# Performance work log

Measured on AMD Instinct MI355X. Metric: run time of the kernel, lower is better.

## Reference

```python
import jax, jax.numpy as jnp
import numpy as np

VOCAB = 50257
HID = 1024


def setup_inputs() -> dict:
    key = jax.random.key(0)
    ks = jax.random.split(key, 9)
    s = 0.05  # weight scale for numerical sanity
    return {
        "input": jax.random.randint(ks[0], (1,), 0, VOCAB),
        "hidden": jax.random.normal(ks[1], (1, 1, HID), jnp.float32),
        "emb": jax.random.normal(ks[2], (VOCAB, HID), jnp.float32) * s,
        "w_ih": jax.random.normal(ks[3], (3 * HID, HID), jnp.float32) * s,
        "w_hh": jax.random.normal(ks[4], (3 * HID, HID), jnp.float32) * s,
        "b_ih": jax.random.normal(ks[5], (3 * HID,), jnp.float32) * s,
        "b_hh": jax.random.normal(ks[6], (3 * HID,), jnp.float32) * s,
        "w_out": jax.random.normal(ks[7], (VOCAB, HID), jnp.float32) * s,
        "b_out": jax.random.normal(ks[8], (VOCAB,), jnp.float32) * s,
    }


def reference(input, hidden, emb, w_ih, w_hh, b_ih, b_hh, w_out, b_out):
    # embedding lookup -> [1, HID], then ReLU
    x = jnp.maximum(emb[input[0]], 0.0)[None, :]          # [1, H]
    h = hidden[0]                                         # [1, H] (layer 0)
    # PyTorch GRU cell, gate order (r, z, n)
    gi = x @ w_ih.T + b_ih                                # [1, 3H]
    gh = h @ w_hh.T + b_hh                                # [1, 3H]
    i_r, i_z, i_n = jnp.split(gi, 3, axis=1)
    h_r, h_z, h_n = jnp.split(gh, 3, axis=1)
    r = jax.nn.sigmoid(i_r + h_r)
    z = jax.nn.sigmoid(i_z + h_z)
    n = jnp.tanh(i_n + r * h_n)
    h_new = (1.0 - z) * n + z * h                         # [1, H]
    # output projection + log-softmax over vocab (dim=1)
    logits = h_new @ w_out.T + b_out                      # [1, V]
    out = jax.nn.log_softmax(logits, axis=1)
    return out, h_new[None, :, :]
```

## Files before the change

kernel.cpp:

```cpp
#include <hip/hip_runtime.h>
#include <hip/hip_bf16.h>
#include <math.h>

#define HID   1024
#define HID3  3072
#define VOCAB 50257

#define LROWS_PER_BLOCK 16
#define LBLOCKS ((VOCAB + LROWS_PER_BLOCK - 1) / LROWS_PER_BLOCK)

#define WS_GI   0
#define WS_GH   3072
#define WS_HN   6144
#define WS_PSUM 7168
#define WS_SCAL 11264

typedef float f32x4 __attribute__((ext_vector_type(4)));

__device__ __forceinline__ float wave_reduce_sum(float s) {
    #pragma unroll
    for (int off = 32; off; off >>= 1) s += __shfl_down(s, off, 64);
    return s;
}

__global__ void gates_kernel(const int* __restrict__ token,
                             const float* __restrict__ emb,
                             const float* __restrict__ w_ih,
                             const float* __restrict__ w_hh,
                             const float* __restrict__ b_ih,
                             const float* __restrict__ b_hh,
                             const float* __restrict__ h,
                             float* __restrict__ gi,
                             float* __restrict__ gh) {
    int gwave = (blockIdx.x * blockDim.x + threadIdx.x) >> 6;
    int lane  = threadIdx.x & 63;
    bool isI  = gwave < HID3;
    int row   = isI ? gwave : gwave - HID3;
    const f32x4* w = (const f32x4*)((isI ? w_ih : w_hh) + (size_t)row * HID);
    float s = 0.0f;
    if (isI) {
        const f32x4* e = (const f32x4*)(emb + (size_t)token[0] * HID);
        #pragma unroll
        for (int it = 0; it < HID / 4 / 64; ++it) {
            f32x4 a = __builtin_nontemporal_load(&w[it * 64 + lane]);
            f32x4 x = e[it * 64 + lane];
            s += a.x * fmaxf(x.x, 0.f) + a.y * fmaxf(x.y, 0.f)
               + a.z * fmaxf(x.z, 0.f) + a.w * fmaxf(x.w, 0.f);
        }
    } else {
        const f32x4* v = (const f32x4*)h;
        #pragma unroll
        for (int it = 0; it < HID / 4 / 64; ++it) {
            f32x4 a = __builtin_nontemporal_load(&w[it * 64 + lane]);
            f32x4 b = v[it * 64 + lane];
            s += a.x * b.x + a.y * b.y + a.z * b.z + a.w * b.w;
        }
    }
    s = wave_reduce_sum(s);
    if (lane == 0) {
        if (isI) gi[row] = s + b_ih[row];
        else     gh[row] = s + b_hh[row];
    }
}

__global__ void hnew_kernel(const float* __restrict__ gi,
                            const float* __restrict__ gh,
                            const float* __restrict__ h,
                            float* __restrict__ hn_ws,
                            float* __restrict__ hn_out) {
    int j = threadIdx.x;
    float r = 1.0f / (1.0f + expf(-(gi[j] + gh[j])));
    float z = 1.0f / (1.0f + expf(-(gi[HID + j] + gh[HID + j])));
    float n = tanhf(gi[2 * HID + j] + r * gh[2 * HID + j]);
    float hv = h[j];
    float hn = (1.0f - z) * n + z * hv;
    hn_ws[j]  = hn;
    hn_out[j] = hn;
}

__global__ void logits_kernel(const float* __restrict__ w_out,
                              const float* __restrict__ b_out,
                              const float* __restrict__ hn,
                              float* __restrict__ out,
                              float* __restrict__ psum) {
    __shared__ f32x4 lh[HID / 4];
    __shared__ float wsum[8];
    int t = threadIdx.x;
    if (t < HID / 4) lh[t] = ((const f32x4*)hn)[t];
    __syncthreads();
    int lane = t & 63, w = t >> 6;
    int r0 = blockIdx.x * LROWS_PER_BLOCK + w * 2;
    int r1 = r0 + 1;
    int c0 = r0 < VOCAB ? r0 : VOCAB - 1;
    int c1 = r1 < VOCAB ? r1 : VOCAB - 1;
    const f32x4* wa = (const f32x4*)(w_out + (size_t)c0 * HID);
    const f32x4* wb = (const f32x4*)(w_out + (size_t)c1 * HID);
    float s0 = 0.0f, s1 = 0.0f;
    #pragma unroll
    for (int it = 0; it < HID / 4 / 64; ++it) {
        f32x4 hv = lh[it * 64 + lane];
        f32x4 a = __builtin_nontemporal_load(&wa[it * 64 + lane]);
        f32x4 b = __builtin_nontemporal_load(&wb[it * 64 + lane]);
        s0 += a.x * hv.x + a.y * hv.y + a.z * hv.z + a.w * hv.w;
        s1 += b.x * hv.x + b.y * hv.y + b.z * hv.z + b.w * hv.w;
    }
    s0 = wave_reduce_sum(s0);
    s1 = wave_reduce_sum(s1);
    if (lane == 0) {
        float e = 0.0f;
        if (r0 < VOCAB) { float l0 = s0 + b_out[r0]; out[r0] = l0; e += expf(l0); }
        if (r1 < VOCAB) { float l1 = s1 + b_out[r1]; out[r1] = l1; e += expf(l1); }
        wsum[w] = e;
    }
    __syncthreads();
    if (t == 0) {
        float tot = 0.0f;
        #pragma unroll
        for (int i = 0; i < 8; ++i) tot += wsum[i];
        psum[blockIdx.x] = tot;
    }
}

__global__ void reduce_kernel(const float* __restrict__ psum,
                              float* __restrict__ scal) {
    __shared__ float wred[16];
    int t = threadIdx.x;
    float s = 0.0f;
    for (int i = t; i < LBLOCKS; i += 1024) s += psum[i];
    s = wave_reduce_sum(s);
    if ((t & 63) == 0) wred[t >> 6] = s;
    __syncthreads();
    if (t == 0) {
        float tot = 0.0f;
        #pragma unroll
        for (int i = 0; i < 16; ++i) tot += wred[i];
        scal[0] = logf(tot);
    }
}

__global__ void final_kernel(float* __restrict__ out,
                             const float* __restrict__ scal) {
    int i = blockIdx.x * 256 + threadIdx.x;
    if (i < VOCAB) out[i] -= scal[0];
}

extern "C" void kernel_launch(void* const* d_in, const int* in_sizes, int n_in,
                              void* d_out, int out_size, void* d_ws, size_t ws_size,
                              hipStream_t stream) {
    const int*   token = (const int*)  d_in[0];
    const float* hidden= (const float*)d_in[1];
    const float* emb   = (const float*)d_in[2];
    const float* w_ih  = (const float*)d_in[3];
    const float* w_hh  = (const float*)d_in[4];
    const float* b_ih  = (const float*)d_in[5];
    const float* b_hh  = (const float*)d_in[6];
    const float* w_out = (const float*)d_in[7];
    const float* b_out = (const float*)d_in[8];

    float* ws  = (float*)d_ws;
    float* out = (float*)d_out;

    float* ws_gi = ws + WS_GI;
    float* ws_gh = ws + WS_GH;
    float* ws_hn = ws + WS_HN;
    float* ws_ps = ws + WS_PSUM;
    float* ws_sc = ws + WS_SCAL;

    gates_kernel<<<768, 512, 0, stream>>>(token, emb, w_ih, w_hh, b_ih, b_hh,
                                          hidden, ws_gi, ws_gh);

    hnew_kernel<<<1, HID, 0, stream>>>(ws_gi, ws_gh, hidden, ws_hn, out + VOCAB);

    logits_kernel<<<LBLOCKS, 512, 0, stream>>>(w_out, b_out, ws_hn, out, ws_ps);

    reduce_kernel<<<1, 1024, 0, stream>>>(ws_ps, ws_sc);

    final_kernel<<<(VOCAB + 255) / 256, 256, 0, stream>>>(out, ws_sc);
}
```

Baseline: 47.66 us.

## Fuse GRU cell update and partial-sum reduction into the logits kernel

Removes the single-block hnew kernel and the reduce kernel. Every logits block now recomputes the GRU h_new from gi/gh into shared memory, and issues its w_out row loads before that work so the loads overlap it. The final softmax normalizer is computed by the last-arriving block, tracked with an atomic counter that the gates kernel resets. The final subtract kernel is also vectorized to four floats per thread. This trades two launches and their serialization gaps for redundant gate math in every block and a threadfence/atomic per block.

Result: slower. 186.1 us (+290.4%).

```diff
diff --git a/kernel.cpp b/kernel.cpp
--- a/kernel.cpp
+++ b/kernel.cpp
@@ -6,14 +6,14 @@
 #define HID3  3072
 #define VOCAB 50257
 
-#define LROWS_PER_BLOCK 16
-#define LBLOCKS ((VOCAB + LROWS_PER_BLOCK - 1) / LROWS_PER_BLOCK)
+#define LROWS   16
+#define LBLOCKS ((VOCAB + LROWS - 1) / LROWS)
 
 #define WS_GI   0
 #define WS_GH   3072
-#define WS_HN   6144
-#define WS_PSUM 7168
-#define WS_SCAL 11264
+#define WS_PSUM 6144
+#define WS_SCAL (6144 + LBLOCKS)
+#define WS_CNT  (6144 + LBLOCKS+1)
 
 typedef float f32x4 __attribute__((ext_vector_type(4)));
 
@@ -31,7 +31,9 @@
                              const float* __restrict__ b_hh,
                              const float* __restrict__ h,
                              float* __restrict__ gi,
-                             float* __restrict__ gh) {
+                             float* __restrict__ gh,
+                             int* __restrict__ cnt) {
+    if (blockIdx.x == 0 && threadIdx.x == 0) cnt[0] = 0;
     int gwave = (blockIdx.x * blockDim.x + threadIdx.x) >> 6;
     int lane  = threadIdx.x & 63;
     bool isI  = gwave < HID3;
@@ -63,46 +65,53 @@
     }
 }
 
-__global__ void hnew_kernel(const float* __restrict__ gi,
-                            const float* __restrict__ gh,
-                            const float* __restrict__ h,
-                            float* __restrict__ hn_ws,
-                            float* __restrict__ hn_out) {
-    int j = threadIdx.x;
-    float r = 1.0f / (1.0f + expf(-(gi[j] + gh[j])));
-    float z = 1.0f / (1.0f + expf(-(gi[HID + j] + gh[HID + j])));
-    float n = tanhf(gi[2 * HID + j] + r * gh[2 * HID + j]);
-    float hv = h[j];
-    float hn = (1.0f - z) * n + z * hv;
-    hn_ws[j]  = hn;
-    hn_out[j] = hn;
-}
-
-__global__ void logits_kernel(const float* __restrict__ w_out,
+__global__ void logits_kernel(const float* __restrict__ gi,
+                              const float* __restrict__ gh,
+                              const float* __restrict__ h,
+                              const float* __restrict__ w_out,
                               const float* __restrict__ b_out,
-                              const float* __restrict__ hn,
                               float* __restrict__ out,
-                              float* __restrict__ psum) {
-    __shared__ f32x4 lh[HID / 4];
+                              float* __restrict__ hn_out,
+                              float* __restrict__ psum,
+                              int* __restrict__ cnt,
+                              float* __restrict__ scal) {
+    __shared__ float lh[HID];
     __shared__ float wsum[8];
-    int t = threadIdx.x;
-    if (t < HID / 4) lh[t] = ((const f32x4*)hn)[t];
-    __syncthreads();
-    int lane = t & 63, w = t >> 6;
-    int r0 = blockIdx.x * LROWS_PER_BLOCK + w * 2;
+    __shared__ int   isLast;
+    int t = threadIdx.x, lane = t & 63, w = t >> 6;
+    int r0 = blockIdx.x * LROWS + w * 2;
     int r1 = r0 + 1;
     int c0 = r0 < VOCAB ? r0 : VOCAB - 1;
     int c1 = r1 < VOCAB ? r1 : VOCAB - 1;
     const f32x4* wa = (const f32x4*)(w_out + (size_t)c0 * HID);
     const f32x4* wb = (const f32x4*)(w_out + (size_t)c1 * HID);
+
+    f32x4 a0[4], a1[4];
+    #pragma unroll
+    for (int k = 0; k < 4; ++k) {
+        a0[k] = __builtin_nontemporal_load(&wa[k * 64 + lane]);
+        a1[k] = __builtin_nontemporal_load(&wb[k * 64 + lane]);
+    }
+
+    #pragma unroll
+    for (int e = 0; e < 2; ++e) {
+        int j = t + e * 512;
+        float r = 1.0f / (1.0f + expf(-(gi[j] + gh[j])));
+        float z = 1.0f / (1.0f + expf(-(gi[HID + j] + gh[HID + j])));
+        float n = tanhf(gi[2 * HID + j] + r * gh[2 * HID + j]);
+        float hn = (1.0f - z) * n + z * h[j];
+        lh[j] = hn;
+        if (blockIdx.x == 0) hn_out[j] = hn;
+    }
+    __syncthreads();
+
+    const f32x4* lhv = (const f32x4*)lh;
     float s0 = 0.0f, s1 = 0.0f;
     #pragma unroll
-    for (int it = 0; it < HID / 4 / 64; ++it) {
-        f32x4 hv = lh[it * 64 + lane];
-        f32x4 a = __builtin_nontemporal_load(&wa[it * 64 + lane]);
-        f32x4 b = __builtin_nontemporal_load(&wb[it * 64 + lane]);
-        s0 += a.x * hv.x + a.y * hv.y + a.z * hv.z + a.w * hv.w;
-        s1 += b.x * hv.x + b.y * hv.y + b.z * hv.z + b.w * hv.w;
+    for (int k = 0; k < 4; ++k) {
+        f32x4 hv = lhv[k * 64 + lane];
+        s0 += a0[k].x * hv.x + a0[k].y * hv.y + a0[k].z * hv.z + a0[k].w * hv.w;
+        s1 += a1[k].x * hv.x + a1[k].y * hv.y + a1[k].z * hv.z + a1[k].w * hv.w;
     }
     s0 = wave_reduce_sum(s0);
     s1 = wave_reduce_sum(s1);
@@ -118,30 +127,40 @@
         #pragma unroll
         for (int i = 0; i < 8; ++i) tot += wsum[i];
         psum[blockIdx.x] = tot;
+        __threadfence();
+        int old = atomicAdd(cnt, 1);
+        isLast = (old == LBLOCKS - 1) ? 1 : 0;
     }
-}
-
-__global__ void reduce_kernel(const float* __restrict__ psum,
-                              float* __restrict__ scal) {
-    __shared__ float wred[16];
-    int t = threadIdx.x;
-    float s = 0.0f;
-    for (int i = t; i < LBLOCKS; i += 1024) s += psum[i];
-    s = wave_reduce_sum(s);
-    if ((t & 63) == 0) wred[t >> 6] = s;
     __syncthreads();
-    if (t == 0) {
-        float tot = 0.0f;
-        #pragma unroll
-        for (int i = 0; i < 16; ++i) tot += wred[i];
-        scal[0] = logf(tot);
+    if (isLast) {
+        __threadfence();
+        float s = 0.0f;
+        for (int i = t; i < LBLOCKS; i += 512) s += psum[i];
+        s = wave_reduce_sum(s);
+        if (lane == 0) wsum[w] = s;
+        __syncthreads();
+        if (t == 0) {
+            float tot = 0.0f;
+            #pragma unroll
+            for (int i = 0; i < 8; ++i) tot += wsum[i];
+            scal[0] = logf(tot);
+        }
     }
 }
 
 __global__ void final_kernel(float* __restrict__ out,
                              const float* __restrict__ scal) {
-    int i = blockIdx.x * 256 + threadIdx.x;
-    if (i < VOCAB) out[i] -= scal[0];
+    int i = (blockIdx.x * 256 + threadIdx.x) * 4;
+    float l = scal[0];
+    if (i + 3 < VOCAB) {
+        f32x4 v = *(f32x4*)(out + i);
+        v.x -= l; v.y -= l; v.z -= l; v.w -= l;
+        *(f32x4*)(out + i) = v;
+    } else {
+        #pragma unroll
+        for (int k = 0; k < 4; ++k)
+            if (i + k < VOCAB) out[i + k] -= l;
+    }
 }
 
 extern "C" void kernel_launch(void* const* d_in, const int* in_sizes, int n_in,
@@ -162,18 +181,17 @@
 
     float* ws_gi = ws + WS_GI;
     float* ws_gh = ws + WS_GH;
-    float* ws_hn = ws + WS_HN;
     float* ws_ps = ws + WS_PSUM;
     float* ws_sc = ws + WS_SCAL;
+    int*   ws_ct = (int*)(ws + WS_CNT);
 
     gates_kernel<<<768, 512, 0, stream>>>(token, emb, w_ih, w_hh, b_ih, b_hh,
-                                          hidden, ws_gi, ws_gh);
+                                          hidden, ws_gi, ws_gh, ws_ct);
 
-    hnew_kernel<<<1, HID, 0, stream>>>(ws_gi, ws_gh, hidden, ws_hn, out + VOCAB);
+    logits_kernel<<<LBLOCKS, 512, 0, stream>>>(ws_gi, ws_gh, hidden,
+                                               w_out, b_out,
+                                               out, out + VOCAB,
+                                               ws_ps, ws_ct, ws_sc);
 
-    logits_kernel<<<LBLOCKS, 512, 0, stream>>>(w_out, b_out, ws_hn, out, ws_ps);
-
-    reduce_kernel<<<1, 1024, 0, stream>>>(ws_ps, ws_sc);
-
-    final_kernel<<<(VOCAB + 255) / 256, 256, 0, stream>>>(out, ws_sc);
+    final_kernel<<<(VOCAB + 1023) / 1024, 256, 0, stream>>>(out, ws_sc);
 }
```
